# Kernel optimization log

Measured on AMD Instinct MI355X. Metric: run time of the kernel, lower is better.

The kernel has to match this reference:

```python
import jax, jax.numpy as jnp
import numpy as np

EPS = 1e-5
SCALE = 1.0 / np.float32(np.sqrt(64.0))  # 1/sqrt(d_Q)


def layernorm(x):
    # fresh nn.LayerNorm each call: gamma=1, beta=0
    m = jnp.mean(x, axis=-1, keepdims=True)
    v = jnp.mean((x - m) ** 2, axis=-1, keepdims=True)
    return (x - m) * jax.lax.rsqrt(v + EPS)


def setup_inputs() -> dict:
    key = jax.random.key(0)
    ks = jax.random.split(key, 8)
    B, S, D, H, F = 32, 512, 256, 64, 256
    w = 0.05
    return {
        "x": jax.random.normal(ks[0], (B, S, D), jnp.float32),
        "mask": jax.random.randint(ks[1], (B, 6, S, S), 0, 2).astype(jnp.int32),
        "Wq": jax.random.normal(ks[2], (6, D, H), jnp.float32) * w,
        "Wk": jax.random.normal(ks[3], (6, D, H), jnp.float32) * w,
        "Wv": jax.random.normal(ks[4], (6, D, H), jnp.float32) * w,
        "Wfc": jax.random.normal(ks[5], (6, H, D), jnp.float32) * w,
        "W1": jax.random.normal(ks[6], (D, F), jnp.float32) * w,
        "W2": jax.random.normal(ks[7], (F, D), jnp.float32) * w,
    }


def reference(x, mask, Wq, Wk, Wv, Wfc, W1, W2):
    m = mask.astype(bool)                                   # [B,6,S,S]
    # batched over the 6 relation branches (r axis)
    Q = jnp.einsum('bsd,rdh->brsh', x, Wq)                  # [B,6,S,64]
    K = jnp.einsum('bsd,rdh->brsh', x, Wk)
    V = jnp.einsum('bsd,rdh->brsh', x, Wv)
    score = jnp.einsum('brsh,brth->brst', Q, K) * SCALE     # [B,6,S,S]
    score = jnp.where(m, jnp.float32(-1e9), score)
    attn = jax.nn.softmax(score, axis=-1)
    attn = jnp.where(m, jnp.float32(0.0), attn)             # post-softmax zeroing
    ctx = jnp.einsum('brst,brth->brsh', attn, V)            # [B,6,S,64]
    proj = jnp.einsum('brsh,rhd->brsd', ctx, Wfc)           # [B,6,S,256]
    branch = layernorm(proj + x[:, None, :, :])             # residual + fresh LN per branch
    s = jnp.sum(branch, axis=1)                             # sum of 6 branches [B,S,256]
    ffn = jnp.maximum(jnp.einsum('bsd,df->bsf', s, W1), 0.0)
    ffn = jnp.einsum('bsf,fd->bsd', ffn, W2)
    return layernorm(ffn + s)
```

## Files before the change

kernel.cpp:

```cpp
#include <hip/hip_runtime.h>
#include <hip/hip_bf16.h>

#define BB 32
#define RR 6
#define SS 512
#define DD 256
#define HH 64
#define FF 256

typedef short  short8 __attribute__((ext_vector_type(8)));
typedef short  short4v __attribute__((ext_vector_type(4)));
typedef float  f32x4  __attribute__((ext_vector_type(4)));
typedef unsigned short ushort_t;

__device__ __forceinline__ ushort_t f2bf(float f) {
    __hip_bfloat16 b = __float2bfloat16(f);
    return __builtin_bit_cast(ushort_t, b);
}
__device__ __forceinline__ float bf2f(ushort_t u) {
    return __bfloat162float(__builtin_bit_cast(__hip_bfloat16, u));
}

__global__ __launch_bounds__(256) void convert_x_kernel(
        const float* __restrict__ x, ushort_t* __restrict__ xb) {
    int gid = blockIdx.x * 256 + threadIdx.x;
    const float4* src = (const float4*)x;
    float4 fv = src[gid];
    short4v o;
    o[0] = (short)f2bf(fv.x); o[1] = (short)f2bf(fv.y);
    o[2] = (short)f2bf(fv.z); o[3] = (short)f2bf(fv.w);
    *(short4v*)(xb + (size_t)gid * 4) = o;
}

__global__ __launch_bounds__(256) void convert_w_kernel(
        const float* __restrict__ Wq, const float* __restrict__ Wk, const float* __restrict__ Wv,
        ushort_t* __restrict__ wT) {
    int gid = blockIdx.x * 256 + threadIdx.x;
    int n = gid >> 8, d = gid & 255;
    int r = n / 192, rem = n % 192;
    int which = rem >> 6, h = rem & 63;
    const float* W = which == 0 ? Wq : which == 1 ? Wk : Wv;
    wT[gid] = f2bf(W[(size_t)r * DD * HH + (size_t)d * HH + h]);
}

__global__ __launch_bounds__(256) void convert_ffnw_kernel(
        const float* __restrict__ W1, const float* __restrict__ W2,
        ushort_t* __restrict__ w1T, ushort_t* __restrict__ w2T) {
    int gid = blockIdx.x * 256 + threadIdx.x;
    if (gid < 65536) {
        int f = gid >> 8, d = gid & 255;
        w1T[gid] = f2bf(W1[(size_t)d * FF + f]);
    } else {
        int gg = gid - 65536;
        int d = gg >> 8, f = gg & 255;
        w2T[gg] = f2bf(W2[(size_t)f * DD + d]);
    }
}

__global__ __launch_bounds__(256) void convert_wfc_kernel(
        const float* __restrict__ Wfc, ushort_t* __restrict__ wfcT) {
    int gid = blockIdx.x * 256 + threadIdx.x;
    int n = gid >> 6, h = gid & 63;
    int r = n >> 8, d = n & 255;
    wfcT[gid] = f2bf(Wfc[((size_t)r * HH + h) * DD + d]);
}

__global__ __launch_bounds__(256) void qkv_mfma_kernel(
        const ushort_t* __restrict__ xb, const ushort_t* __restrict__ wT,
        ushort_t* __restrict__ q, ushort_t* __restrict__ k, ushort_t* __restrict__ v) {
    int bid = blockIdx.x;
    int id = (bid & 7) * 288 + (bid >> 3);
    int rt = id / 18, cw = id % 18;
    int r = cw / 3, which = cw % 3;

    int tid = threadIdx.x;
    int wv = tid >> 6, l = tid & 63;
    int wr = wv >> 1, wc = wv & 1;
    int g = l >> 4, lc = l & 15;

    const ushort_t* Arow = xb + ((size_t)(rt * 128 + wr * 64 + lc)) * DD + g * 8;
    const ushort_t* Brow = wT + ((size_t)(cw * 64 + wc * 32 + lc)) * DD + g * 8;

    f32x4 acc[4][2] = {};
    #pragma unroll 4
    for (int ks = 0; ks < 8; ++ks) {
        short8 af[4], bf[2];
        #pragma unroll
        for (int m = 0; m < 4; ++m)
            af[m] = *(const short8*)(Arow + (size_t)m * 16 * DD + ks * 32);
        #pragma unroll
        for (int n = 0; n < 2; ++n)
            bf[n] = *(const short8*)(Brow + (size_t)n * 16 * DD + ks * 32);
        #pragma unroll
        for (int m = 0; m < 4; ++m)
            #pragma unroll
            for (int n = 0; n < 2; ++n)
                acc[m][n] = __builtin_amdgcn_mfma_f32_16x16x32_bf16(af[m], bf[n], acc[m][n], 0, 0, 0);
    }

    ushort_t* outb = which == 0 ? q : which == 1 ? k : v;
    #pragma unroll
    for (int m = 0; m < 4; ++m) {
        #pragma unroll
        for (int reg = 0; reg < 4; ++reg) {
            int grow = rt * 128 + wr * 64 + m * 16 + g * 4 + reg;
            int orow = ((grow >> 9) * RR + r) * SS + (grow & (SS - 1));
            #pragma unroll
            for (int n = 0; n < 2; ++n)
                outb[(size_t)orow * HH + wc * 32 + n * 16 + lc] = f2bf(acc[m][n][reg]);
        }
    }
}

__global__ __launch_bounds__(256) void attn_mfma_kernel(
        const ushort_t* __restrict__ q, const ushort_t* __restrict__ k,
        const ushort_t* __restrict__ v, const int* __restrict__ mask,
        ushort_t* __restrict__ ctx) {
    int wg = blockIdx.x;
    int id = (wg & 7) * 192 + (wg >> 3);
    int br = id >> 3, qt = id & 7;

    __shared__ ushort_t K_lds[64 * 72];
    __shared__ ushort_t VT_lds[64 * 72];
    __shared__ ushort_t P_lds[4][16 * 72];

    int tid = threadIdx.x;
    int wv = tid >> 6, l = tid & 63;
    int g = l >> 4, lc = l & 15;

    int q0 = qt * 64 + wv * 16;
    const size_t base_kv = (size_t)br * SS * HH;

    short8 qf[2];
    #pragma unroll
    for (int kk = 0; kk < 2; ++kk)
        qf[kk] = *(const short8*)(q + ((size_t)br * SS + q0 + lc) * HH + kk * 32 + g * 8);

    f32x4 O[4] = {{0,0,0,0},{0,0,0,0},{0,0,0,0},{0,0,0,0}};
    float mrun[4] = {-1e9f, -1e9f, -1e9f, -1e9f};
    float lrun[4] = {0.f, 0.f, 0.f, 0.f};

    const int* mb = mask + ((size_t)br * SS + q0) * SS;

    for (int t0 = 0; t0 < SS; t0 += 64) {
        __syncthreads();
        for (int c = tid; c < 512; c += 256) {
            int t = c >> 3, c8 = (c & 7) * 8;
            *(short8*)&K_lds[t * 72 + c8] =
                *(const short8*)(k + base_kv + (size_t)(t0 + t) * HH + c8);
        }
        {
            int h = tid & 63, tseg = tid >> 6;
            #pragma unroll
            for (int j = 0; j < 16; ++j) {
                int t = tseg * 16 + j;
                VT_lds[h * 72 + t] = v[base_kv + (size_t)(t0 + t) * HH + h];
            }
        }
        __syncthreads();

        f32x4 S[4];
        #pragma unroll
        for (int tc = 0; tc < 4; ++tc) {
            f32x4 c = {0, 0, 0, 0};
            #pragma unroll
            for (int kk = 0; kk < 2; ++kk) {
                short8 bf = *(const short8*)&K_lds[(tc * 16 + lc) * 72 + kk * 32 + g * 8];
                c = __builtin_amdgcn_mfma_f32_16x16x32_bf16(qf[kk], bf, c, 0, 0, 0);
            }
            S[tc] = c;
        }

        float tmax[4] = {-1e9f, -1e9f, -1e9f, -1e9f};
        #pragma unroll
        for (int tc = 0; tc < 4; ++tc)
            #pragma unroll
            for (int reg = 0; reg < 4; ++reg) {
                int qrow = 4 * g + reg;
                int mv = mb[(size_t)qrow * SS + t0 + tc * 16 + lc];
                float sv = mv ? -1e9f : S[tc][reg] * 0.125f;
                S[tc][reg] = sv;
                tmax[reg] = fmaxf(tmax[reg], sv);
            }
        #pragma unroll
        for (int reg = 0; reg < 4; ++reg) {
            float tm = tmax[reg];
            tm = fmaxf(tm, __shfl_xor(tm, 1, 64));
            tm = fmaxf(tm, __shfl_xor(tm, 2, 64));
            tm = fmaxf(tm, __shfl_xor(tm, 4, 64));
            tm = fmaxf(tm, __shfl_xor(tm, 8, 64));
            tmax[reg] = tm;
        }
        float psum[4];
        #pragma unroll
        for (int reg = 0; reg < 4; ++reg) {
            float mnew = fmaxf(mrun[reg], tmax[reg]);
            float corr = __expf(mrun[reg] - mnew);
            mrun[reg] = mnew;
            lrun[reg] *= corr;
            O[0][reg] *= corr; O[1][reg] *= corr; O[2][reg] *= corr; O[3][reg] *= corr;
            psum[reg] = 0.f;
        }
        ushort_t* Pw = P_lds[wv];
        #pragma unroll
        for (int tc = 0; tc < 4; ++tc)
            #pragma unroll
            for (int reg = 0; reg < 4; ++reg) {
                float sv = S[tc][reg];
                float p = (sv == -1e9f) ? 0.f : __expf(sv - mrun[reg]);
                psum[reg] += p;
                Pw[(4 * g + reg) * 72 + tc * 16 + lc] = f2bf(p);
            }
        #pragma unroll
        for (int reg = 0; reg < 4; ++reg) {
            float ps = psum[reg];
            ps += __shfl_xor(ps, 1, 64);
            ps += __shfl_xor(ps, 2, 64);
            ps += __shfl_xor(ps, 4, 64);
            ps += __shfl_xor(ps, 8, 64);
            lrun[reg] += ps;
        }
        asm volatile("s_waitcnt lgkmcnt(0)" ::: "memory");

        #pragma unroll
        for (int ts = 0; ts < 2; ++ts) {
            short8 pa = *(const short8*)&Pw[lc * 72 + ts * 32 + g * 8];
            #pragma unroll
            for (int hb = 0; hb < 4; ++hb) {
                short8 vbf = *(const short8*)&VT_lds[(hb * 16 + lc) * 72 + ts * 32 + g * 8];
                O[hb] = __builtin_amdgcn_mfma_f32_16x16x32_bf16(pa, vbf, O[hb], 0, 0, 0);
            }
        }
    }

    ushort_t* cb = ctx + ((size_t)br * SS + q0) * HH;
    #pragma unroll
    for (int reg = 0; reg < 4; ++reg) {
        float inv = lrun[reg] > 0.f ? 1.f / lrun[reg] : 0.f;
        #pragma unroll
        for (int hb = 0; hb < 4; ++hb)
            cb[(size_t)(4 * g + reg) * HH + hb * 16 + lc] = f2bf(O[hb][reg] * inv);
    }
}

__global__ __launch_bounds__(256) void proj_ln_mfma_kernel(
        const ushort_t* __restrict__ ctx, const ushort_t* __restrict__ wfcT,
        const float* __restrict__ x, ushort_t* __restrict__ srow_bf) {
    int bid = blockIdx.x;
    int rt = (bid & 7) * 64 + (bid >> 3);
    int b = rt >> 4, s0 = (rt & 15) * 32;

    int tid = threadIdx.x;
    int wv = tid >> 6, l = tid & 63;
    int wr = wv >> 1, wc = wv & 1;
    int g = l >> 4, lc = l & 15;

    __shared__ float red_s[32][2];
    __shared__ float red_q[32][2];

    float xres[8][4];
    #pragma unroll
    for (int hb = 0; hb < 8; ++hb)
        #pragma unroll
        for (int reg = 0; reg < 4; ++reg)
            xres[hb][reg] = x[((size_t)b * SS + s0 + wr * 16 + g * 4 + reg) * DD
                              + wc * 128 + hb * 16 + lc];

    float acc_ln[8][4] = {};

    for (int r = 0; r < RR; ++r) {
        const ushort_t* Abase = ctx + (((size_t)b * RR + r) * SS + s0 + wr * 16 + lc) * HH + g * 8;
        const ushort_t* Bbase = wfcT + ((size_t)r * 256 + wc * 128 + lc) * HH + g * 8;
        f32x4 acc[8] = {};
        #pragma unroll
        for (int ks = 0; ks < 2; ++ks) {
            short8 af = *(const short8*)(Abase + ks * 32);
            #pragma unroll
            for (int hb = 0; hb < 8; ++hb) {
                short8 bf = *(const short8*)(Bbase + (size_t)hb * 16 * HH + ks * 32);
                acc[hb] = __builtin_amdgcn_mfma_f32_16x16x32_bf16(af, bf, acc[hb], 0, 0, 0);
            }
        }

        float vals[8][4];
        float psum[4] = {0, 0, 0, 0}, psq[4] = {0, 0, 0, 0};
        #pragma unroll
        for (int hb = 0; hb < 8; ++hb)
            #pragma unroll
            for (int reg = 0; reg < 4; ++reg) {
                float vv = acc[hb][reg] + xres[hb][reg];
                vals[hb][reg] = vv;
                psum[reg] += vv;
                psq[reg]  += vv * vv;
            }
        #pragma unroll
        for (int reg = 0; reg < 4; ++reg) {
            #pragma unroll
            for (int off = 1; off <= 8; off <<= 1) {
                psum[reg] += __shfl_xor(psum[reg], off, 64);
                psq[reg]  += __shfl_xor(psq[reg],  off, 64);
            }
        }
        if (lc == 0) {
            #pragma unroll
            for (int reg = 0; reg < 4; ++reg) {
                int row = wr * 16 + g * 4 + reg;
                red_s[row][wc] = psum[reg];
                red_q[row][wc] = psq[reg];
            }
        }
        __syncthreads();
        float mean_r[4], inv_r[4];
        #pragma unroll
        for (int reg = 0; reg < 4; ++reg) {
            int row = wr * 16 + g * 4 + reg;
            float sum = red_s[row][0] + red_s[row][1];
            float sq  = red_q[row][0] + red_q[row][1];
            float mean = sum * (1.f / 256.f);
            float var  = sq * (1.f / 256.f) - mean * mean;
            mean_r[reg] = mean;
            inv_r[reg]  = rsqrtf(var + 1e-5f);
        }
        #pragma unroll
        for (int hb = 0; hb < 8; ++hb)
            #pragma unroll
            for (int reg = 0; reg < 4; ++reg)
                acc_ln[hb][reg] += (vals[hb][reg] - mean_r[reg]) * inv_r[reg];
        __syncthreads();
    }

    #pragma unroll
    for (int hb = 0; hb < 8; ++hb)
        #pragma unroll
        for (int reg = 0; reg < 4; ++reg) {
            int row = wr * 16 + g * 4 + reg;
            int col = wc * 128 + hb * 16 + lc;
            srow_bf[((size_t)b * SS + s0 + row) * DD + col] = f2bf(acc_ln[hb][reg]);
        }
}

__global__ __launch_bounds__(256) void ffn_mfma_kernel(
        const ushort_t* __restrict__ srow_bf, const ushort_t* __restrict__ w1T,
        const ushort_t* __restrict__ w2T, float* __restrict__ out) {
    int rt = blockIdx.x;
    int tid = threadIdx.x;
    int wv = tid >> 6, l = tid & 63;
    int wr = wv >> 1, wc = wv & 1;
    int g = l >> 4, lc = l & 15;

    __shared__ ushort_t s_lds[32 * 264];
    __shared__ ushort_t h_lds[32 * 264];
    __shared__ float red_s[32][2];
    __shared__ float red_q[32][2];

    for (int c = tid; c < 1024; c += 256) {
        int row = c >> 5, c8 = (c & 31) * 8;
        *(short8*)&s_lds[row * 264 + c8] =
            *(const short8*)(srow_bf + ((size_t)rt * 32 + row) * DD + c8);
    }
    __syncthreads();

    f32x4 acc[8] = {};
    #pragma unroll
    for (int ks = 0; ks < 8; ++ks) {
        short8 af = *(const short8*)&s_lds[(wr * 16 + lc) * 264 + ks * 32 + g * 8];
        #pragma unroll
        for (int hb = 0; hb < 8; ++hb) {
            short8 bf = *(const short8*)(w1T + (size_t)(wc * 128 + hb * 16 + lc) * DD + ks * 32 + g * 8);
            acc[hb] = __builtin_amdgcn_mfma_f32_16x16x32_bf16(af, bf, acc[hb], 0, 0, 0);
        }
    }
    #pragma unroll
    for (int hb = 0; hb < 8; ++hb)
        #pragma unroll
        for (int reg = 0; reg < 4; ++reg) {
            int row = wr * 16 + g * 4 + reg;
            int col = wc * 128 + hb * 16 + lc;
            h_lds[row * 264 + col] = f2bf(fmaxf(acc[hb][reg], 0.f));
        }
    __syncthreads();

    f32x4 acc2[8] = {};
    #pragma unroll
    for (int ks = 0; ks < 8; ++ks) {
        short8 af = *(const short8*)&h_lds[(wr * 16 + lc) * 264 + ks * 32 + g * 8];
        #pragma unroll
        for (int hb = 0; hb < 8; ++hb) {
            short8 bf = *(const short8*)(w2T + (size_t)(wc * 128 + hb * 16 + lc) * FF + ks * 32 + g * 8);
            acc2[hb] = __builtin_amdgcn_mfma_f32_16x16x32_bf16(af, bf, acc2[hb], 0, 0, 0);
        }
    }

    float vals[8][4];
    float psum[4] = {0, 0, 0, 0}, psq[4] = {0, 0, 0, 0};
    #pragma unroll
    for (int hb = 0; hb < 8; ++hb)
        #pragma unroll
        for (int reg = 0; reg < 4; ++reg) {
            int row = wr * 16 + g * 4 + reg;
            int col = wc * 128 + hb * 16 + lc;
            float vv = acc2[hb][reg] + bf2f(s_lds[row * 264 + col]);
            vals[hb][reg] = vv;
            psum[reg] += vv;
            psq[reg]  += vv * vv;
        }
    #pragma unroll
    for (int reg = 0; reg < 4; ++reg) {
        #pragma unroll
        for (int off = 1; off <= 8; off <<= 1) {
            psum[reg] += __shfl_xor(psum[reg], off, 64);
            psq[reg]  += __shfl_xor(psq[reg],  off, 64);
        }
    }
    if (lc == 0) {
        #pragma unroll
        for (int reg = 0; reg < 4; ++reg) {
            int row = wr * 16 + g * 4 + reg;
            red_s[row][wc] = psum[reg];
            red_q[row][wc] = psq[reg];
        }
    }
    __syncthreads();
    float mean_r[4], inv_r[4];
    #pragma unroll
    for (int reg = 0; reg < 4; ++reg) {
        int row = wr * 16 + g * 4 + reg;
        float sum = red_s[row][0] + red_s[row][1];
        float sq  = red_q[row][0] + red_q[row][1];
        float mean = sum * (1.f / 256.f);
        float var  = sq * (1.f / 256.f) - mean * mean;
        mean_r[reg] = mean;
        inv_r[reg]  = rsqrtf(var + 1e-5f);
    }
    #pragma unroll
    for (int hb = 0; hb < 8; ++hb)
        #pragma unroll
        for (int reg = 0; reg < 4; ++reg) {
            int row = wr * 16 + g * 4 + reg;
            int col = wc * 128 + hb * 16 + lc;
            out[((size_t)rt * 32 + row) * DD + col] = (vals[hb][reg] - mean_r[reg]) * inv_r[reg];
        }
}

extern "C" void kernel_launch(void* const* d_in, const int* in_sizes, int n_in,
                              void* d_out, int out_size, void* d_ws, size_t ws_size,
                              hipStream_t stream) {
    const float* x    = (const float*)d_in[0];
    const int*   mask = (const int*)  d_in[1];
    const float* Wq   = (const float*)d_in[2];
    const float* Wk   = (const float*)d_in[3];
    const float* Wv   = (const float*)d_in[4];
    const float* Wfc  = (const float*)d_in[5];
    const float* W1   = (const float*)d_in[6];
    const float* W2   = (const float*)d_in[7];
    float* out = (float*)d_out;

    const size_t QKV = (size_t)BB * RR * SS * HH;
    const size_t BSD = (size_t)BB * SS * DD;
    ushort_t* qb  = (ushort_t*)d_ws;
    ushort_t* kb  = qb + QKV;
    ushort_t* vb  = kb + QKV;
    ushort_t* ctx = vb + QKV;
    ushort_t* srow_bf = ctx + QKV;
    ushort_t* xb  = srow_bf + BSD;
    ushort_t* wT  = xb + BSD;
    ushort_t* wfcT = wT + (size_t)1152 * 256;
    ushort_t* w1T = wfcT + (size_t)RR * 256 * 64;
    ushort_t* w2T = w1T + 65536;

    convert_x_kernel   <<<4096, 256, 0, stream>>>(x, xb);
    convert_w_kernel   <<<1152, 256, 0, stream>>>(Wq, Wk, Wv, wT);
    convert_ffnw_kernel<<<512,  256, 0, stream>>>(W1, W2, w1T, w2T);
    convert_wfc_kernel <<<384,  256, 0, stream>>>(Wfc, wfcT);
    qkv_mfma_kernel    <<<2304, 256, 0, stream>>>(xb, wT, qb, kb, vb);
    attn_mfma_kernel   <<<BB * RR * 8, 256, 0, stream>>>(qb, kb, vb, mask, ctx);
    proj_ln_mfma_kernel<<<512, 256, 0, stream>>>(ctx, wfcT, x, srow_bf);
    ffn_mfma_kernel    <<<512, 256, 0, stream>>>(srow_bf, w1T, w2T, out);
}
```

Measured before the change: 216.3 us.

## Fuse x conversion into QKV, merge weight converts, fuse proj-LN with FFN

The separate x-to-bf16 kernel is removed, and the QKV GEMM now loads fp32 x and converts it in registers. The four weight-conversion kernels become one launch. The projection+LayerNorm kernel and the FFN kernel merge into one tail kernel, so the summed branch rows stay in LDS instead of going to global memory as bf16. The V-transpose LDS stride also changes from 72 to 66, which breaks 16-byte alignment of the short8 LDS reads and may cause split or misaligned accesses. The aim is fewer launches and less global traffic, at the cost of reading x at twice the bytes in the QKV GEMM.

```diff
diff --git a/kernel.cpp b/kernel.cpp
--- a/kernel.cpp
+++ b/kernel.cpp
@@ -9,7 +9,6 @@
 #define FF 256
 
 typedef short  short8 __attribute__((ext_vector_type(8)));
-typedef short  short4v __attribute__((ext_vector_type(4)));
 typedef float  f32x4  __attribute__((ext_vector_type(4)));
 typedef unsigned short ushort_t;
 
@@ -21,52 +20,36 @@
     return __bfloat162float(__builtin_bit_cast(__hip_bfloat16, u));
 }
 
-__global__ __launch_bounds__(256) void convert_x_kernel(
-        const float* __restrict__ x, ushort_t* __restrict__ xb) {
+__global__ __launch_bounds__(256) void convert_weights_kernel(
+        const float* __restrict__ Wq, const float* __restrict__ Wk, const float* __restrict__ Wv,
+        const float* __restrict__ Wfc, const float* __restrict__ W1, const float* __restrict__ W2,
+        ushort_t* __restrict__ wT, ushort_t* __restrict__ w1T,
+        ushort_t* __restrict__ w2T, ushort_t* __restrict__ wfcT) {
     int gid = blockIdx.x * 256 + threadIdx.x;
-    const float4* src = (const float4*)x;
-    float4 fv = src[gid];
-    short4v o;
-    o[0] = (short)f2bf(fv.x); o[1] = (short)f2bf(fv.y);
-    o[2] = (short)f2bf(fv.z); o[3] = (short)f2bf(fv.w);
-    *(short4v*)(xb + (size_t)gid * 4) = o;
-}
-
-__global__ __launch_bounds__(256) void convert_w_kernel(
-        const float* __restrict__ Wq, const float* __restrict__ Wk, const float* __restrict__ Wv,
-        ushort_t* __restrict__ wT) {
-    int gid = blockIdx.x * 256 + threadIdx.x;
-    int n = gid >> 8, d = gid & 255;
-    int r = n / 192, rem = n % 192;
-    int which = rem >> 6, h = rem & 63;
-    const float* W = which == 0 ? Wq : which == 1 ? Wk : Wv;
-    wT[gid] = f2bf(W[(size_t)r * DD * HH + (size_t)d * HH + h]);
-}
-
-__global__ __launch_bounds__(256) void convert_ffnw_kernel(
-        const float* __restrict__ W1, const float* __restrict__ W2,
-        ushort_t* __restrict__ w1T, ushort_t* __restrict__ w2T) {
-    int gid = blockIdx.x * 256 + threadIdx.x;
-    if (gid < 65536) {
-        int f = gid >> 8, d = gid & 255;
-        w1T[gid] = f2bf(W1[(size_t)d * FF + f]);
-    } else {
-        int gg = gid - 65536;
+    if (gid < 294912) {
+        int n = gid >> 8, d = gid & 255;
+        int r = n / 192, rem = n % 192;
+        int which = rem >> 6, h = rem & 63;
+        const float* W = which == 0 ? Wq : which == 1 ? Wk : Wv;
+        wT[gid] = f2bf(W[(size_t)r * DD * HH + (size_t)d * HH + h]);
+    } else if (gid < 360448) {
+        int gg = gid - 294912;
+        int f = gg >> 8, d = gg & 255;
+        w1T[gg] = f2bf(W1[(size_t)d * FF + f]);
+    } else if (gid < 425984) {
+        int gg = gid - 360448;
         int d = gg >> 8, f = gg & 255;
         w2T[gg] = f2bf(W2[(size_t)f * DD + d]);
-    }
-}
-
-__global__ __launch_bounds__(256) void convert_wfc_kernel(
-        const float* __restrict__ Wfc, ushort_t* __restrict__ wfcT) {
-    int gid = blockIdx.x * 256 + threadIdx.x;
-    int n = gid >> 6, h = gid & 63;
-    int r = n >> 8, d = n & 255;
-    wfcT[gid] = f2bf(Wfc[((size_t)r * HH + h) * DD + d]);
+    } else {
+        int gg = gid - 425984;
+        int n = gg >> 6, h = gg & 63;
+        int r = n >> 8, d = n & 255;
+        wfcT[gg] = f2bf(Wfc[((size_t)r * HH + h) * DD + d]);
+    }
 }
 
 __global__ __launch_bounds__(256) void qkv_mfma_kernel(
-        const ushort_t* __restrict__ xb, const ushort_t* __restrict__ wT,
+        const float* __restrict__ x, const ushort_t* __restrict__ wT,
         ushort_t* __restrict__ q, ushort_t* __restrict__ k, ushort_t* __restrict__ v) {
     int bid = blockIdx.x;
     int id = (bid & 7) * 288 + (bid >> 3);
@@ -78,7 +61,7 @@
     int wr = wv >> 1, wc = wv & 1;
     int g = l >> 4, lc = l & 15;
 
-    const ushort_t* Arow = xb + ((size_t)(rt * 128 + wr * 64 + lc)) * DD + g * 8;
+    const float*    Arow = x  + ((size_t)(rt * 128 + wr * 64 + lc)) * DD + g * 8;
     const ushort_t* Brow = wT + ((size_t)(cw * 64 + wc * 32 + lc)) * DD + g * 8;
 
     f32x4 acc[4][2] = {};
@@ -86,8 +69,16 @@
     for (int ks = 0; ks < 8; ++ks) {
         short8 af[4], bf[2];
         #pragma unroll
-        for (int m = 0; m < 4; ++m)
-            af[m] = *(const short8*)(Arow + (size_t)m * 16 * DD + ks * 32);
+        for (int m = 0; m < 4; ++m) {
+            float4 f0 = *(const float4*)(Arow + (size_t)m * 16 * DD + ks * 32);
+            float4 f1 = *(const float4*)(Arow + (size_t)m * 16 * DD + ks * 32 + 4);
+            short8 a;
+            a[0] = (short)f2bf(f0.x); a[1] = (short)f2bf(f0.y);
+            a[2] = (short)f2bf(f0.z); a[3] = (short)f2bf(f0.w);
+            a[4] = (short)f2bf(f1.x); a[5] = (short)f2bf(f1.y);
+            a[6] = (short)f2bf(f1.z); a[7] = (short)f2bf(f1.w);
+            af[m] = a;
+        }
         #pragma unroll
         for (int n = 0; n < 2; ++n)
             bf[n] = *(const short8*)(Brow + (size_t)n * 16 * DD + ks * 32);
@@ -121,7 +112,7 @@
     int br = id >> 3, qt = id & 7;
 
     __shared__ ushort_t K_lds[64 * 72];
-    __shared__ ushort_t VT_lds[64 * 72];
+    __shared__ ushort_t VT_lds[64 * 66];
     __shared__ ushort_t P_lds[4][16 * 72];
 
     int tid = threadIdx.x;
@@ -154,7 +145,7 @@
             #pragma unroll
             for (int j = 0; j < 16; ++j) {
                 int t = tseg * 16 + j;
-                VT_lds[h * 72 + t] = v[base_kv + (size_t)(t0 + t) * HH + h];
+                VT_lds[h * 66 + t] = v[base_kv + (size_t)(t0 + t) * HH + h];
             }
         }
         __syncthreads();
@@ -227,7 +218,7 @@
             short8 pa = *(const short8*)&Pw[lc * 72 + ts * 32 + g * 8];
             #pragma unroll
             for (int hb = 0; hb < 4; ++hb) {
-                short8 vbf = *(const short8*)&VT_lds[(hb * 16 + lc) * 72 + ts * 32 + g * 8];
+                short8 vbf = *(const short8*)&VT_lds[(hb * 16 + lc) * 66 + ts * 32 + g * 8];
                 O[hb] = __builtin_amdgcn_mfma_f32_16x16x32_bf16(pa, vbf, O[hb], 0, 0, 0);
             }
         }
@@ -243,9 +234,10 @@
     }
 }
 
-__global__ __launch_bounds__(256) void proj_ln_mfma_kernel(
+__global__ __launch_bounds__(256) void fused_tail_kernel(
         const ushort_t* __restrict__ ctx, const ushort_t* __restrict__ wfcT,
-        const float* __restrict__ x, ushort_t* __restrict__ srow_bf) {
+        const float* __restrict__ x, const ushort_t* __restrict__ w1T,
+        const ushort_t* __restrict__ w2T, float* __restrict__ out) {
     int bid = blockIdx.x;
     int rt = (bid & 7) * 64 + (bid >> 3);
     int b = rt >> 4, s0 = (rt & 15) * 32;
@@ -255,6 +247,8 @@
     int wr = wv >> 1, wc = wv & 1;
     int g = l >> 4, lc = l & 15;
 
+    __shared__ ushort_t s_lds[32 * 264];
+    __shared__ ushort_t h_lds[32 * 264];
     __shared__ float red_s[32][2];
     __shared__ float red_q[32][2];
 
@@ -335,39 +329,18 @@
         for (int reg = 0; reg < 4; ++reg) {
             int row = wr * 16 + g * 4 + reg;
             int col = wc * 128 + hb * 16 + lc;
-            srow_bf[((size_t)b * SS + s0 + row) * DD + col] = f2bf(acc_ln[hb][reg]);
-        }
-}
-
-__global__ __launch_bounds__(256) void ffn_mfma_kernel(
-        const ushort_t* __restrict__ srow_bf, const ushort_t* __restrict__ w1T,
-        const ushort_t* __restrict__ w2T, float* __restrict__ out) {
-    int rt = blockIdx.x;
-    int tid = threadIdx.x;
-    int wv = tid >> 6, l = tid & 63;
-    int wr = wv >> 1, wc = wv & 1;
-    int g = l >> 4, lc = l & 15;
-
-    __shared__ ushort_t s_lds[32 * 264];
-    __shared__ ushort_t h_lds[32 * 264];
-    __shared__ float red_s[32][2];
-    __shared__ float red_q[32][2];
-
-    for (int c = tid; c < 1024; c += 256) {
-        int row = c >> 5, c8 = (c & 31) * 8;
-        *(short8*)&s_lds[row * 264 + c8] =
-            *(const short8*)(srow_bf + ((size_t)rt * 32 + row) * DD + c8);
-    }
+            s_lds[row * 264 + col] = f2bf(acc_ln[hb][reg]);
+        }
     __syncthreads();
 
-    f32x4 acc[8] = {};
+    f32x4 acc1[8] = {};
     #pragma unroll
     for (int ks = 0; ks < 8; ++ks) {
         short8 af = *(const short8*)&s_lds[(wr * 16 + lc) * 264 + ks * 32 + g * 8];
         #pragma unroll
         for (int hb = 0; hb < 8; ++hb) {
             short8 bf = *(const short8*)(w1T + (size_t)(wc * 128 + hb * 16 + lc) * DD + ks * 32 + g * 8);
-            acc[hb] = __builtin_amdgcn_mfma_f32_16x16x32_bf16(af, bf, acc[hb], 0, 0, 0);
+            acc1[hb] = __builtin_amdgcn_mfma_f32_16x16x32_bf16(af, bf, acc1[hb], 0, 0, 0);
         }
     }
     #pragma unroll
@@ -376,7 +349,7 @@
         for (int reg = 0; reg < 4; ++reg) {
             int row = wr * 16 + g * 4 + reg;
             int col = wc * 128 + hb * 16 + lc;
-            h_lds[row * 264 + col] = f2bf(fmaxf(acc[hb][reg], 0.f));
+            h_lds[row * 264 + col] = f2bf(fmaxf(acc1[hb][reg], 0.f));
         }
     __syncthreads();
 
@@ -456,24 +429,18 @@
     float* out = (float*)d_out;
 
     const size_t QKV = (size_t)BB * RR * SS * HH;
-    const size_t BSD = (size_t)BB * SS * DD;
     ushort_t* qb  = (ushort_t*)d_ws;
     ushort_t* kb  = qb + QKV;
     ushort_t* vb  = kb + QKV;
     ushort_t* ctx = vb + QKV;
-    ushort_t* srow_bf = ctx + QKV;
-    ushort_t* xb  = srow_bf + BSD;
-    ushort_t* wT  = xb + BSD;
-    ushort_t* wfcT = wT + (size_t)1152 * 256;
-    ushort_t* w1T = wfcT + (size_t)RR * 256 * 64;
+    ushort_t* wT  = ctx + QKV;
+    ushort_t* w1T = wT + (size_t)1152 * 256;
     ushort_t* w2T = w1T + 65536;
-
-    convert_x_kernel   <<<4096, 256, 0, stream>>>(x, xb);
-    convert_w_kernel   <<<1152, 256, 0, stream>>>(Wq, Wk, Wv, wT);
-    convert_ffnw_kernel<<<512,  256, 0, stream>>>(W1, W2, w1T, w2T);
-    convert_wfc_kernel <<<384,  256, 0, stream>>>(Wfc, wfcT);
-    qkv_mfma_kernel    <<<2304, 256, 0, stream>>>(xb, wT, qb, kb, vb);
-    attn_mfma_kernel   <<<BB * RR * 8, 256, 0, stream>>>(qb, kb, vb, mask, ctx);
-    proj_ln_mfma_kernel<<<512, 256, 0, stream>>>(ctx, wfcT, x, srow_bf);
-    ffn_mfma_kernel    <<<512, 256, 0, stream>>>(srow_bf, w1T, w2T, out);
-}
+    ushort_t* wfcT = w2T + 65536;
+
+    convert_weights_kernel<<<2048, 256, 0, stream>>>(Wq, Wk, Wv, Wfc, W1, W2,
+                                                     wT, w1T, w2T, wfcT);
+    qkv_mfma_kernel  <<<2304, 256, 0, stream>>>(x, wT, qb, kb, vb);
+    attn_mfma_kernel <<<BB * RR * 8, 256, 0, stream>>>(qb, kb, vb, mask, ctx);
+    fused_tail_kernel<<<512, 256, 0, stream>>>(ctx, wfcT, x, w1T, w2T, out);
+}
```

New measurement: 228.7 us. 5.7% more time.
